# Kernel tuning notes

Hardware: AMD Instinct MI355X
Metric: run time of the kernel (lower is better)

Reference implementation:

```python
import jax, jax.numpy as jnp
import numpy as np

N = 50000
D_IN = 512
D_HID = 2048
N_CLS = 40
E = 200000


def setup_inputs() -> dict:
    key = jax.random.key(0)
    ks = jax.random.split(key, 8)
    x = jax.random.normal(ks[0], (N, D_IN), dtype=jnp.float32)
    edge_index = jax.random.randint(ks[1], (2, E), 0, N, dtype=jnp.int32)
    # GCNConv weights (glorot-ish scale) and biases
    W1 = jax.random.normal(ks[2], (D_IN, D_HID), dtype=jnp.float32) / np.sqrt(D_IN)
    b1 = jnp.zeros((D_HID,), dtype=jnp.float32)
    W2 = jax.random.normal(ks[3], (D_HID, D_HID), dtype=jnp.float32) / np.sqrt(D_HID)
    b2 = jnp.zeros((D_HID,), dtype=jnp.float32)
    W3 = jax.random.normal(ks[4], (D_HID, N_CLS), dtype=jnp.float32) / np.sqrt(D_HID)
    b3 = jnp.zeros((N_CLS,), dtype=jnp.float32)
    return {"x": x, "edge_index": edge_index, "W1": W1, "b1": b1,
            "W2": W2, "b2": b2, "W3": W3, "b3": b3}


def _gcn_conv(x, src, dst, deg_norm, W, b, n):
    # PyG GCNConv: transform first, then normalized sum-aggregate, then bias.
    h = x @ W                              # [N, out]
    msg = h[src] * deg_norm[:, None]       # [E+N, out] gather + edge normalize
    out = jax.ops.segment_sum(msg, dst, num_segments=n)  # scatter-add
    return out + b


def _pairnorm(x, scale=1.0, eps=1e-6):
    # PyG PairNorm (scale_individually=False): center cols, rescale by mean row norm.
    xc = x - x.mean(axis=0, keepdims=True)
    denom = jnp.sqrt(eps + (xc * xc).sum(axis=-1).mean())
    return scale * xc / denom


def _edges_with_self_loops_and_norm(edge_index, n):
    loop = jnp.arange(n, dtype=edge_index.dtype)
    src = jnp.concatenate([edge_index[0], loop])
    dst = jnp.concatenate([edge_index[1], loop])
    deg = jax.ops.segment_sum(jnp.ones_like(dst, dtype=jnp.float32), dst, num_segments=n)
    dinv = jnp.where(deg > 0, jax.lax.rsqrt(jnp.maximum(deg, 1.0)), 0.0)
    norm = dinv[src] * dinv[dst]           # D^{-1/2} (A+I) D^{-1/2} edge weights
    return src, dst, norm


def reference(x, edge_index, W1, b1, W2, b2, W3, b3):
    n = x.shape[0]
    # drop_edge keep_ratio=1.0 keeps all edges -> identity
    src, dst, norm = _edges_with_self_loops_and_norm(edge_index, n)
    h = _gcn_conv(x, src, dst, norm, W1, b1, n)
    h = jax.nn.relu(_pairnorm(h))
    h = _gcn_conv(h, src, dst, norm, W2, b2, n)
    h = jax.nn.relu(_pairnorm(h))
    out = _gcn_conv(h, src, dst, norm, W3, b3, n)
    return out
```

## Files before the change

### kernel.cpp

```cpp
#include <hip/hip_runtime.h>
#include <cstdint>
#include <cstddef>

using f32x4 = __attribute__((ext_vector_type(4))) float;
using short8 = __attribute__((ext_vector_type(8))) short;

__device__ __forceinline__ float blo(unsigned int u) { return __uint_as_float(u << 16); }
__device__ __forceinline__ float bhi(unsigned int u) { return __uint_as_float(u & 0xffff0000u); }
__device__ __forceinline__ unsigned short f2b(float f) {
  unsigned int i = __float_as_uint(f);
  return (unsigned short)((i + 0x7fffu + ((i >> 16) & 1u)) >> 16);
}
__device__ __forceinline__ unsigned int packb2(float a, float b) {
  return (unsigned int)f2b(a) | ((unsigned int)f2b(b) << 16);
}
__device__ __forceinline__ void gload_lds16(const void* g, void* l) {
  typedef __attribute__((address_space(1))) const unsigned int gui_t;
  typedef __attribute__((address_space(3))) unsigned int lui_t;
  __builtin_amdgcn_global_load_lds((gui_t*)(uintptr_t)g, (lui_t*)(uintptr_t)l, 16, 0, 0);
}
__device__ __forceinline__ void xcd_remap(int gx, int gy, int& bx, int& by) {
  int nwg = gx * gy;
  int flat = by * gx + bx;
  int q = nwg >> 3, rmd = nwg & 7;
  int xcd = flat & 7, pos = flat >> 3;
  int base = (xcd < rmd) ? xcd * (q + 1) : rmd * (q + 1) + (xcd - rmd) * q;
  int nf = base + pos;
  bx = nf % gx;
  by = nf / gx;
}

__global__ void k_sentinel(float* out, long long total, float v) {
  long long i = (long long)blockIdx.x * blockDim.x + threadIdx.x;
  long long stride = (long long)gridDim.x * blockDim.x;
  for (; i < total; i += stride) out[i] = v;
}

__global__ void k_init_deg(int* deg, int n) {
  int i = blockIdx.x * blockDim.x + threadIdx.x;
  if (i < n) deg[i] = 1;
}
__global__ void k_count(const int* __restrict__ ei, int* __restrict__ deg, int e) {
  int i = blockIdx.x * blockDim.x + threadIdx.x;
  if (i < e) atomicAdd(&deg[ei[e + i]], 1);
}
__global__ void k_dinv(const int* __restrict__ deg, float* __restrict__ dinv, int n) {
  int i = blockIdx.x * blockDim.x + threadIdx.x;
  if (i < n) dinv[i] = rsqrtf((float)deg[i]);
}
__global__ void k_scan(const int* __restrict__ deg, int* __restrict__ offs, int n) {
  __shared__ int sums[1024];
  int tid = threadIdx.x;
  int chunk = (n + 1023) / 1024;
  int s0 = tid * chunk, s1 = s0 + chunk;
  if (s1 > n) s1 = n;
  if (s0 > n) s0 = n;
  int s = 0;
  for (int i = s0; i < s1; i++) s += deg[i];
  sums[tid] = s;
  __syncthreads();
  if (tid == 0) {
    int acc = 0;
    for (int i = 0; i < 1024; i++) { int v = sums[i]; sums[i] = acc; acc += v; }
  }
  __syncthreads();
  int off = sums[tid];
  for (int i = s0; i < s1; i++) { offs[i] = off; off += deg[i]; }
  if (tid == 1023) offs[n] = off;
}
__global__ void k_copy_int(int* __restrict__ dst, const int* __restrict__ src, int n) {
  int i = blockIdx.x * blockDim.x + threadIdx.x;
  if (i < n) dst[i] = src[i];
}
__global__ void k_copy_u4(uint4* __restrict__ dst, const uint4* __restrict__ src, int n16) {
  int i = blockIdx.x * blockDim.x + threadIdx.x;
  int stride = gridDim.x * blockDim.x;
  for (; i < n16; i += stride) dst[i] = src[i];
}
__global__ void k_fill_edges(const int* __restrict__ ei, int e, int* __restrict__ cursor,
                             unsigned short* __restrict__ colv) {
  int i = blockIdx.x * blockDim.x + threadIdx.x;
  if (i < e) {
    int s = ei[i], d = ei[e + i];
    int pos = atomicAdd(&cursor[d], 1);
    colv[pos] = (unsigned short)s;
  }
}
__global__ void k_fill_loops(int* __restrict__ cursor, unsigned short* __restrict__ colv, int n) {
  int i = blockIdx.x * blockDim.x + threadIdx.x;
  if (i < n) {
    int pos = atomicAdd(&cursor[i], 1);
    colv[pos] = (unsigned short)i;
  }
}

__global__ void k_cvt_bf16(const float2* __restrict__ in, unsigned int* __restrict__ out, long long total) {
  long long i = (long long)blockIdx.x * blockDim.x + threadIdx.x;
  long long stride = (long long)gridDim.x * blockDim.x;
  for (; i < total; i += stride) {
    float2 v = in[i];
    out[i] = packb2(v.x, v.y);
  }
}
__global__ void k_transpose_cvt(const float* __restrict__ in, unsigned short* __restrict__ out,
                                int K, int M, int Mout) {
  __shared__ float tile[32][33];
  int kb = blockIdx.x * 32;
  int mb = blockIdx.y * 32;
  int tx = threadIdx.x, ty = threadIdx.y;
#pragma unroll
  for (int j = 0; j < 4; j++) {
    int k = kb + ty + j * 8, m = mb + tx;
    tile[ty + j * 8][tx] = (k < K && m < M) ? in[(size_t)k * M + m] : 0.0f;
  }
  __syncthreads();
#pragma unroll
  for (int j = 0; j < 4; j++) {
    int m = mb + ty + j * 8, k = kb + tx;
    if (m < Mout && k < K) out[(size_t)m * K + k] = f2b(tile[tx][ty + j * 8]);
  }
}

__global__ void k_aggregate_512(const unsigned int* __restrict__ in, unsigned short* __restrict__ out,
                                const int* __restrict__ offs, const unsigned short* __restrict__ colv,
                                const float* __restrict__ dinv) {
  int i = blockIdx.x;
  int tid = threadIdx.x;
  float di = dinv[i];
  int p0 = offs[i], p1 = offs[i + 1];
  float a0 = 0.f, a1 = 0.f;
  for (int p = p0; p < p1; p++) {
    int c = (int)colv[p];
    float wgt = dinv[c] * di;
    unsigned int u = in[(size_t)c * 256 + tid];
    a0 += wgt * blo(u); a1 += wgt * bhi(u);
  }
  ((unsigned int*)out)[(size_t)i * 256 + tid] = packb2(a0, a1);
}

__global__ void k_aggregate_pn(const unsigned short* __restrict__ in, unsigned short* __restrict__ outws,
                               unsigned short* __restrict__ outtail, int rsplit,
                               const int* __restrict__ offs, const unsigned short* __restrict__ colv,
                               const float* __restrict__ dinv, const float* __restrict__ meanv,
                               const float* __restrict__ scalev) {
  int i = blockIdx.x;
  int tid = threadIdx.x;
  float di = dinv[i];
  float s = scalev[0];
  float m[8];
#pragma unroll
  for (int j = 0; j < 8; j++) m[j] = meanv[tid * 8 + j];
  int p0 = offs[i], p1 = offs[i + 1];
  const uint4* inv = (const uint4*)in;
  float a[8] = {};
  for (int p = p0; p < p1; p++) {
    int c = (int)colv[p];
    float wgt = dinv[c] * di;
    uint4 u = inv[(size_t)c * 256 + tid];
    a[0] += wgt * fmaxf((blo(u.x) - m[0]) * s, 0.f);
    a[1] += wgt * fmaxf((bhi(u.x) - m[1]) * s, 0.f);
    a[2] += wgt * fmaxf((blo(u.y) - m[2]) * s, 0.f);
    a[3] += wgt * fmaxf((bhi(u.y) - m[3]) * s, 0.f);
    a[4] += wgt * fmaxf((blo(u.z) - m[4]) * s, 0.f);
    a[5] += wgt * fmaxf((bhi(u.z) - m[5]) * s, 0.f);
    a[6] += wgt * fmaxf((blo(u.w) - m[6]) * s, 0.f);
    a[7] += wgt * fmaxf((bhi(u.w) - m[7]) * s, 0.f);
  }
  uint4 o;
  o.x = packb2(a[0], a[1]); o.y = packb2(a[2], a[3]);
  o.z = packb2(a[4], a[5]); o.w = packb2(a[6], a[7]);
  char* base = (i < rsplit) ? (char*)outws + (size_t)i * 4096
                            : (char*)outtail + (size_t)(i - rsplit) * 4096;
  ((uint4*)base)[tid] = o;
}

template <int MQ>
__device__ __forceinline__ void load_a(const char* ldsA, short8 (&a)[4][2], int wm, int lane) {
  const int frow = lane & 15;
  const int cb0 = (lane >> 4) << 4;
  const int xorb = (lane & 7) << 4;
#pragma unroll
  for (int i = 0; i < 4; i++)
#pragma unroll
    for (int kk = 0; kk < 2; kk++)
      a[i][kk] = *(const short8*)(ldsA + (wm * 128 + MQ * 64 + i * 16 + frow) * 128 +
                                  ((kk * 64 + cb0) ^ xorb));
}
template <int NQ>
__device__ __forceinline__ void load_b(const char* ldsB, short8 (&b)[2][2][2], int wn, int lane) {
  const int frow = lane & 15;
  const int cb0 = (lane >> 4) << 4;
  const int xorb = (lane & 7) << 4;
#pragma unroll
  for (int j = 0; j < 2; j++)
#pragma unroll
    for (int kk = 0; kk < 2; kk++)
      b[NQ][j][kk] = *(const short8*)(ldsB + (wn * 64 + NQ * 32 + j * 16 + frow) * 128 +
                                      ((kk * 64 + cb0) ^ xorb));
}
template <int MQ, int NQ>
__device__ __forceinline__ void mfma_q(short8 (&a)[4][2], short8 (&b)[2][2][2], f32x4 (&acc)[8][4]) {
  __builtin_amdgcn_s_setprio(1);
#pragma unroll
  for (int i = 0; i < 4; i++)
#pragma unroll
    for (int j = 0; j < 2; j++)
#pragma unroll
      for (int kk = 0; kk < 2; kk++)
        acc[MQ * 4 + i][NQ * 2 + j] =
            __builtin_amdgcn_mfma_f32_16x16x32_bf16(a[i][kk], b[NQ][j][kk], acc[MQ * 4 + i][NQ * 2 + j], 0, 0, 0);
  __builtin_amdgcn_s_setprio(0);
}

__global__ __launch_bounds__(512, 2) void k_gemm256(const unsigned short* __restrict__ A,
                                                    const char* __restrict__ a_tail, int rsplit,
                                                    const unsigned short* __restrict__ BT,
                                                    const float* __restrict__ bias,
                                                    float* __restrict__ colsum, float* __restrict__ ssq,
                                                    unsigned short* __restrict__ Cout,
                                                    int M, int K, int Nout, int m_base) {
  __shared__ __align__(16) char smem[131072];
  const int t = threadIdx.x;
  const int lane = t & 63;
  const int wid = t >> 6;
  const int wm = wid >> 2, wn = wid & 3;
  int bx = blockIdx.x, by = blockIdx.y;
  xcd_remap(gridDim.x, gridDim.y, bx, by);
  const int n0 = bx * 256;
  const int m0 = m_base + by * 256;
  const size_t rowK = (size_t)K * 2;
  const int NT = K >> 6;

  const int rA = t >> 3;
  const int colS = (((t & 7) ^ ((t >> 3) & 7)) << 4);

  auto rowptrA = [&](int r) -> const char* {
    int gr = m0 + r; if (gr >= M) gr = M - 1;
    return (gr < rsplit ? (const char*)A + (size_t)gr * rowK
                        : a_tail + (size_t)(gr - rsplit) * rowK) + colS;
  };
  const char* sA00 = rowptrA(rA);
  const char* sA01 = rowptrA(128 + rA);
  const char* sA10 = rowptrA(64 + rA);
  const char* sA11 = rowptrA(192 + rA);
  const int rbl = (t >> 8) * 64 + ((t >> 3) & 31);
  const int rB00 = rbl, rB01 = 128 + rbl;
  const int rB10 = 32 + rbl, rB11 = 160 + rbl;
  const char* sB00 = (const char*)BT + (size_t)(n0 + rB00) * rowK + colS;
  const char* sB01 = (const char*)BT + (size_t)(n0 + rB01) * rowK + colS;
  const char* sB10 = (const char*)BT + (size_t)(n0 + rB10) * rowK + colS;
  const char* sB11 = (const char*)BT + (size_t)(n0 + rB11) * rowK + colS;
  const int t16 = t * 16;
  const int dA00 = t16, dA01 = 16384 + t16, dA10 = 8192 + t16, dA11 = 24576 + t16;
  const int c7 = (t & 7) * 16;
  const int dB00 = 32768 + rB00 * 128 + c7, dB01 = 32768 + rB01 * 128 + c7;
  const int dB10 = 32768 + rB10 * 128 + c7, dB11 = 32768 + rB11 * 128 + c7;

  f32x4 acc[8][4] = {};
  short8 a[4][2], b[2][2][2];

  gload_lds16(sA00, smem + dA00); gload_lds16(sA01, smem + dA01);
  gload_lds16(sA10, smem + dA10); gload_lds16(sA11, smem + dA11);
  gload_lds16(sB00, smem + dB00); gload_lds16(sB01, smem + dB01);
  gload_lds16(sB10, smem + dB10); gload_lds16(sB11, smem + dB11);
  gload_lds16(sA00 + 128, smem + 65536 + dA00); gload_lds16(sA01 + 128, smem + 65536 + dA01);
  gload_lds16(sA10 + 128, smem + 65536 + dA10); gload_lds16(sA11 + 128, smem + 65536 + dA11);
  sA00 += 256; sA01 += 256; sA10 += 256; sA11 += 256;
  sB00 += 128; sB01 += 128; sB10 += 128; sB11 += 128;
  asm volatile("s_waitcnt vmcnt(4)" ::: "memory");
  asm volatile("s_barrier" ::: "memory");
  load_a<0>((const char*)smem, a, wm, lane);
  load_b<0>((const char*)smem + 32768, b, wn, lane);

  for (int kt = 0; kt < NT; ++kt) {
    const int cbo = (kt & 1) << 16;
    const int sbo = cbo ^ 65536;
    const char* LA = (const char*)smem + cbo;
    const char* LB = LA + 32768;
    const char* NA = (const char*)smem + sbo;
    const char* NB = NA + 32768;
    char* SB = smem + sbo;
    char* SA = smem + cbo;
    gload_lds16(sB00, SB + dB00); gload_lds16(sB01, SB + dB01);
    asm volatile("s_waitcnt vmcnt(6)" ::: "memory");
    asm volatile("s_barrier" ::: "memory");
    mfma_q<0, 0>(a, b, acc);
    load_b<1>(LB, b, wn, lane);
    __builtin_amdgcn_sched_barrier(0);
    asm volatile("s_barrier" ::: "memory");
    gload_lds16(sB10, SB + dB10); gload_lds16(sB11, SB + dB11);
    asm volatile("s_barrier" ::: "memory");
    mfma_q<0, 1>(a, b, acc);
    load_a<1>(LA, a, wm, lane);
    __builtin_amdgcn_sched_barrier(0);
    asm volatile("s_barrier" ::: "memory");
    gload_lds16(sA00, SA + dA00); gload_lds16(sA01, SA + dA01);
    asm volatile("s_barrier" ::: "memory");
    mfma_q<1, 0>(a, b, acc);
    __builtin_amdgcn_sched_barrier(0);
    asm volatile("s_barrier" ::: "memory");
    gload_lds16(sA10, SA + dA10); gload_lds16(sA11, SA + dA11);
    asm volatile("s_waitcnt vmcnt(6)" ::: "memory");
    asm volatile("s_barrier" ::: "memory");
    mfma_q<1, 1>(a, b, acc);
    load_a<0>(NA, a, wm, lane);
    load_b<0>(NB, b, wn, lane);
    __builtin_amdgcn_sched_barrier(0);
    asm volatile("s_barrier" ::: "memory");
    sA00 += 128; sA01 += 128; sA10 += 128; sA11 += 128;
    sB00 += 128; sB01 += 128; sB10 += 128; sB11 += 128;
  }

  const int rrow = (lane >> 4) * 4;
  const int ccol = lane & 15;
  float ss = 0.f;
  float csum[4] = {0.f, 0.f, 0.f, 0.f};
#pragma unroll
  for (int f = 0; f < 8; f++) {
#pragma unroll
    for (int g = 0; g < 4; g++) {
      int col = n0 + wn * 64 + g * 16 + ccol;
      float bv = bias[col];
#pragma unroll
      for (int r = 0; r < 4; r++) {
        int row = m0 + wm * 128 + f * 16 + rrow + r;
        if (row < M) {
          float v = acc[f][g][r] + bv;
          Cout[(size_t)row * Nout + col] = f2b(v);
          csum[g] += v; ss += v * v;
        }
      }
    }
  }
#pragma unroll
  for (int g = 0; g < 4; g++) {
    float w = csum[g];
    w += __shfl_xor(w, 16);
    w += __shfl_xor(w, 32);
    if (lane < 16) atomicAdd(&colsum[n0 + wn * 64 + g * 16 + lane], w);
  }
  for (int mk = 32; mk >= 1; mk >>= 1) ss += __shfl_xor(ss, mk);
  if (lane == 0) atomicAdd(ssq, ss);
}

template <int BM, int BN, int WAVES_M, int WAVES_N, bool ADD_BIAS, bool OUT_BF16, bool STATS>
__global__ __launch_bounds__(256) void k_gemm_bf16(const unsigned short* __restrict__ A,
                                                   const char* __restrict__ a_tail, int rsplit,
                                                   const unsigned short* __restrict__ BT,
                                                   const float* __restrict__ bias,
                                                   float* __restrict__ colsum, float* __restrict__ ssq,
                                                   void* __restrict__ Cout,
                                                   int M, int K, int Nout, int m_base) {
  constexpr int BK = 64;
  constexpr int FM = BM / (WAVES_M * 16);
  constexpr int FN = BN / (WAVES_N * 16);
  __shared__ unsigned short lA[BM * BK];
  __shared__ unsigned short lB[BN * BK];
  const int tid = threadIdx.x;
  const int lane = tid & 63;
  const int wid = tid >> 6;
  int bx = blockIdx.x, by = blockIdx.y;
  xcd_remap(gridDim.x, gridDim.y, bx, by);
  const int n0 = bx * BN;
  const int m0 = m_base + by * BM;
  const int wrow = (wid / WAVES_N) * (FM * 16);
  const int wcol = (wid % WAVES_N) * (FN * 16);
  constexpr int ABYTES = BM * BK * 2;
  constexpr int BBYTES = BN * BK * 2;
  constexpr int ACH = ABYTES / 4096;
  constexpr int BCH = BBYTES / 4096;
  const size_t rowbytes = (size_t)K * 2;

  f32x4 acc[FM][FN] = {};
  const int frow = lane & 15;
  const int kcol8 = (lane >> 4) * 8;
  const int xorb = (lane & 7) << 4;

  for (int k0 = 0; k0 < K; k0 += BK) {
#pragma unroll
    for (int c = 0; c < ACH; c++) {
      int o = wid * (ABYTES / 4) + c * 1024 + lane * 16;
      int r = o >> 7;
      int kbs = (o & 127) ^ ((r & 7) << 4);
      int gr = m0 + r; if (gr >= M) gr = M - 1;
      const char* rowp = (gr < rsplit) ? (const char*)A + (size_t)gr * rowbytes
                                       : a_tail + (size_t)(gr - rsplit) * rowbytes;
      gload_lds16(rowp + (size_t)k0 * 2 + kbs, (char*)lA + o);
    }
#pragma unroll
    for (int c = 0; c < BCH; c++) {
      int o = wid * (BBYTES / 4) + c * 1024 + lane * 16;
      int r = o >> 7;
      int kbs = (o & 127) ^ ((r & 7) << 4);
      gload_lds16((const char*)BT + (size_t)(n0 + r) * rowbytes + (size_t)k0 * 2 + kbs, (char*)lB + o);
    }
    __syncthreads();
#pragma unroll
    for (int kk = 0; kk < BK; kk += 32) {
      short8 af[FM], bfr[FN];
#pragma unroll
      for (int t = 0; t < FM; t++)
        af[t] = *(const short8*)((const char*)lA + (wrow + t * 16 + frow) * 128 +
                                 (((kk + kcol8) * 2) ^ xorb));
#pragma unroll
      for (int u = 0; u < FN; u++)
        bfr[u] = *(const short8*)((const char*)lB + (wcol + u * 16 + frow) * 128 +
                                  (((kk + kcol8) * 2) ^ xorb));
#pragma unroll
      for (int t = 0; t < FM; t++)
#pragma unroll
        for (int u = 0; u < FN; u++)
          acc[t][u] = __builtin_amdgcn_mfma_f32_16x16x32_bf16(af[t], bfr[u], acc[t][u], 0, 0, 0);
    }
    __syncthreads();
  }

  const int rrow = (lane >> 4) * 4;
  const int ccol = lane & 15;
  float ss = 0.f;
  float ca[FN];
#pragma unroll
  for (int u = 0; u < FN; u++) ca[u] = 0.f;
#pragma unroll
  for (int t = 0; t < FM; t++) {
#pragma unroll
    for (int u = 0; u < FN; u++) {
#pragma unroll
      for (int r = 0; r < 4; r++) {
        int row = m0 + wrow + t * 16 + rrow + r;
        int col = n0 + wcol + u * 16 + ccol;
        if (row < M && col < Nout) {
          float v = acc[t][u][r];
          if constexpr (ADD_BIAS) v += bias[col];
          if constexpr (OUT_BF16)
            ((unsigned short*)Cout)[(size_t)row * Nout + col] = f2b(v);
          else
            ((float*)Cout)[(size_t)row * Nout + col] = v;
          if constexpr (STATS) { ca[u] += v; ss += v * v; }
        }
      }
    }
  }
  if constexpr (STATS) {
#pragma unroll
    for (int u = 0; u < FN; u++) {
      float w = ca[u];
      w += __shfl_xor(w, 16);
      w += __shfl_xor(w, 32);
      if (lane < 16) atomicAdd(&colsum[n0 + wcol + u * 16 + lane], w);
    }
    for (int mk = 32; mk >= 1; mk >>= 1) ss += __shfl_xor(ss, mk);
    if (lane == 0) atomicAdd(ssq, ss);
  }
}

__global__ void k_zero(float* p, int n) {
  int i = blockIdx.x * blockDim.x + threadIdx.x;
  if (i < n) p[i] = 0.f;
}
__global__ void k_finalize(const float* __restrict__ colsum, const float* __restrict__ ssq,
                           float* __restrict__ meanv, float* __restrict__ scalev, int nrows, int ncols) {
  __shared__ float red[1024];
  int tid = threadIdx.x;
  float m2 = 0.f;
  for (int c = tid; c < ncols; c += 1024) {
    float m = colsum[c] / (float)nrows;
    meanv[c] = m;
    m2 += m * m;
  }
  red[tid] = m2;
  __syncthreads();
  for (int s = 512; s > 0; s >>= 1) {
    if (tid < s) red[tid] += red[tid + s];
    __syncthreads();
  }
  if (tid == 0) {
    float sstot = ssq[0] - (float)nrows * red[0];
    scalev[0] = rsqrtf(1e-6f + sstot / (float)nrows);
  }
}
__global__ void k_apply_pn_relu(unsigned int* __restrict__ h, const float* __restrict__ meanv,
                                const float* __restrict__ scalev, long long total, int ucolmask) {
  float s = scalev[0];
  long long i = (long long)blockIdx.x * blockDim.x + threadIdx.x;
  long long stride = (long long)gridDim.x * blockDim.x;
  for (; i < total; i += stride) {
    unsigned int u = h[i];
    int cp = (int)(i & ucolmask);
    float a = (blo(u) - meanv[2 * cp]) * s;
    float b = (bhi(u) - meanv[2 * cp + 1]) * s;
    h[i] = packb2(fmaxf(a, 0.f), fmaxf(b, 0.f));
  }
}

__global__ void k_aggregate_out(const float* __restrict__ t, const int* __restrict__ offs,
                                const unsigned short* __restrict__ colv, const float* __restrict__ dinv,
                                const float* __restrict__ b3, float* __restrict__ outp, int ncls) {
  int i = blockIdx.x;
  int j = threadIdx.x;
  if (j < ncls) {
    float di = dinv[i];
    float acc = b3[j];
    for (int p = offs[i]; p < offs[i + 1]; p++) {
      int c = (int)colv[p];
      acc += dinv[c] * di * t[(size_t)c * ncls + j];
    }
    outp[(size_t)i * ncls + j] = acc;
  }
}

extern "C" void kernel_launch(void* const* d_in, const int* in_sizes, int n_in,
                              void* d_out, int out_size, void* d_ws, size_t ws_size,
                              hipStream_t stream) {
  (void)n_in;
  const float* x = (const float*)d_in[0];
  const int* ei = (const int*)d_in[1];
  const float* W1 = (const float*)d_in[2];
  const float* b1 = (const float*)d_in[3];
  const float* W2 = (const float*)d_in[4];
  const float* b2 = (const float*)d_in[5];
  const float* W3 = (const float*)d_in[6];
  const float* b3 = (const float*)d_in[7];
  const int DI = 512, DH = 2048, NC = 40;
  const int n = in_sizes[0] / DI;
  const int e = in_sizes[1] / 2;

  const size_t BIG1B = (size_t)n * DH * 2;
  char* BIG1 = (char*)d_ws;
  char* BIG2 = (char*)d_ws + BIG1B;

  char* dob = (char*)d_out;
  int* deg = (int*)(dob + 0);
  float* dinv = (float*)(dob + 200064);
  int* offs = (int*)(dob + 400128);
  unsigned short* colv = (unsigned short*)(dob + 600192);
  float* colsum = (float*)(dob + 1100288);
  float* meanv = (float*)(dob + 1108480);
  float* ssq = (float*)(dob + 1116672);
  float* scalev = (float*)(dob + 1116928);
  char* aggtail = dob + 2097152;

  long long rows_ws = (long long)(ws_size - BIG1B) / (DH * 2);
  int rsplit = (rows_ws > n) ? n : (int)rows_ws;

  if (ws_size < 403800000UL || rsplit < 48560) {
    float v = (float)(double)(ws_size >> 20);
    k_sentinel<<<512, 256, 0, stream>>>((float*)d_out, (long long)out_size, v);
    return;
  }

  const int W2ROW0 = 47952;
  unsigned short* WT2 = (unsigned short*)(BIG1 + (size_t)W2ROW0 * 4096);
  const int PH2_MBASE = 47872;
  const int PH2_TILES = (n - PH2_MBASE + 255) / 256;

  unsigned short* agg1 = (unsigned short*)BIG2;
  unsigned short* xb = (unsigned short*)(BIG2 + 64000000);
  unsigned short* WT1 = (unsigned short*)(BIG2 + 120000000);
  unsigned short* agg2 = (unsigned short*)BIG2;
  unsigned short* WT2c = (unsigned short*)BIG2;
  float* tbuf = (float*)BIG2;
  unsigned short* WT3 = (unsigned short*)(BIG2 + 9000000);
  int* offs_c = (int*)(BIG2 + 10000000);
  unsigned short* colv_c = (unsigned short*)(BIG2 + 11000000);
  float* dinv_c = (float*)(BIG2 + 12000000);

  dim3 b256(256);
  dim3 b512(512);
  int gn = (n + 255) / 256, ge = (e + 255) / 256;

  k_init_deg<<<gn, b256, 0, stream>>>(deg, n);
  k_count<<<ge, b256, 0, stream>>>(ei, deg, e);
  k_dinv<<<gn, b256, 0, stream>>>(deg, dinv, n);
  k_scan<<<1, 1024, 0, stream>>>(deg, offs, n);
  k_copy_int<<<gn, b256, 0, stream>>>(deg, offs, n);
  k_fill_edges<<<ge, b256, 0, stream>>>(ei, e, deg, colv);
  k_fill_loops<<<gn, b256, 0, stream>>>(deg, colv, n);

  dim3 tb(32, 8);

  k_cvt_bf16<<<2048, b256, 0, stream>>>((const float2*)x, (unsigned int*)xb, (long long)n * DI / 2);
  k_aggregate_512<<<n, b256, 0, stream>>>((const unsigned int*)xb, agg1, offs, colv, dinv);
  k_transpose_cvt<<<dim3(DI / 32, DH / 32), tb, 0, stream>>>(W1, WT1, DI, DH, DH);
  k_zero<<<(DH + 255) / 256, b256, 0, stream>>>(colsum, DH);
  k_zero<<<1, b256, 0, stream>>>(ssq, 1);
  k_gemm256<<<dim3(DH / 256, (n + 255) / 256), b512, 0, stream>>>(
      agg1, (const char*)agg1, n, WT1, b1, colsum, ssq, (unsigned short*)BIG1, n, DI, DH, 0);
  k_finalize<<<1, 1024, 0, stream>>>(colsum, ssq, meanv, scalev, n, DH);

  k_aggregate_pn<<<n, b256, 0, stream>>>((const unsigned short*)BIG1, agg2, (unsigned short*)aggtail,
                                         rsplit, offs, colv, dinv, meanv, scalev);
  k_transpose_cvt<<<dim3(DH / 32, DH / 32), tb, 0, stream>>>(W2, WT2, DH, DH, DH);
  k_zero<<<(DH + 255) / 256, b256, 0, stream>>>(colsum, DH);
  k_zero<<<1, b256, 0, stream>>>(ssq, 1);
  k_gemm256<<<dim3(DH / 256, 187), b512, 0, stream>>>(
      agg2, aggtail, rsplit, WT2, b2, colsum, ssq, (unsigned short*)BIG1, n, DH, DH, 0);
  k_copy_u4<<<2048, b256, 0, stream>>>((uint4*)WT2c, (const uint4*)WT2, (int)(8388608 / 16));
  k_gemm256<<<dim3(DH / 256, PH2_TILES), b512, 0, stream>>>(
      agg2, aggtail, rsplit, WT2c, b2, colsum, ssq, (unsigned short*)BIG1, n, DH, DH, PH2_MBASE);
  k_finalize<<<1, 1024, 0, stream>>>(colsum, ssq, meanv, scalev, n, DH);
  k_apply_pn_relu<<<2048, b256, 0, stream>>>((unsigned int*)BIG1, meanv, scalev, (long long)n * DH / 2, DH / 2 - 1);

  k_transpose_cvt<<<dim3(DH / 32, 2), tb, 0, stream>>>(W3, WT3, DH, NC, 64);
  k_gemm_bf16<128, 64, 4, 1, false, false, false><<<dim3(1, (n + 127) / 128), b256, 0, stream>>>(
      (const unsigned short*)BIG1, BIG1, n, WT3, nullptr, nullptr, nullptr, tbuf, n, DH, NC, 0);
  k_copy_int<<<(n + 256) / 256, b256, 0, stream>>>(offs_c, offs, n + 1);
  k_copy_int<<<((e + n) / 2 + 255) / 256, b256, 0, stream>>>((int*)colv_c, (const int*)colv, (e + n) / 2);
  k_copy_int<<<gn, b256, 0, stream>>>((int*)dinv_c, (const int*)dinv, n);
  k_aggregate_out<<<n, 64, 0, stream>>>(tbuf, offs_c, colv_c, dinv_c, b3, (float*)d_out, NC);
}
```

Baseline: 1.403 ms.

## Fuse PairNorm+ReLU into final GEMM A-load and merge small launches

Drops the separate full-tensor PairNorm/ReLU pass over the N×2048 bf16 hidden activations. The normalization is instead applied while the layer-3 GEMM loads its A tiles into LDS, using a new 64-row-tile kernel. It also merges the stats-zeroing and three metadata copy kernels into single launches, makes finalize reset the accumulators, and packs four nodes per block in the output aggregation. The A path now uses register loads plus VALU conversion instead of direct global-to-LDS loads, which may reduce load overlap in the final GEMM.

```diff
diff --git a/kernel.cpp b/kernel.cpp
--- a/kernel.cpp
+++ b/kernel.cpp
@@ -92,6 +92,15 @@
     int pos = atomicAdd(&cursor[i], 1);
     colv[pos] = (unsigned short)i;
   }
+}
+__global__ void k_copy_meta(const int* __restrict__ offs, int* __restrict__ offs_c,
+                            const int* __restrict__ colv, int* __restrict__ colv_c, int colv_ints,
+                            const float* __restrict__ dinv, float* __restrict__ dinv_c, int n) {
+  int i = blockIdx.x * blockDim.x + threadIdx.x;
+  int stride = gridDim.x * blockDim.x;
+  for (int k = i; k <= n; k += stride) offs_c[k] = offs[k];
+  for (int k = i; k < colv_ints; k += stride) colv_c[k] = colv[k];
+  for (int k = i; k < n; k += stride) dinv_c[k] = dinv[k];
 }
 
 __global__ void k_cvt_bf16(const float2* __restrict__ in, unsigned int* __restrict__ out, long long total) {
@@ -343,122 +352,87 @@
   if (lane == 0) atomicAdd(ssq, ss);
 }
 
-template <int BM, int BN, int WAVES_M, int WAVES_N, bool ADD_BIAS, bool OUT_BF16, bool STATS>
-__global__ __launch_bounds__(256) void k_gemm_bf16(const unsigned short* __restrict__ A,
-                                                   const char* __restrict__ a_tail, int rsplit,
-                                                   const unsigned short* __restrict__ BT,
-                                                   const float* __restrict__ bias,
-                                                   float* __restrict__ colsum, float* __restrict__ ssq,
-                                                   void* __restrict__ Cout,
-                                                   int M, int K, int Nout, int m_base) {
+__global__ __launch_bounds__(256) void k_gemm3_pn(const unsigned short* __restrict__ A,
+                                                  const float* __restrict__ meanv,
+                                                  const float* __restrict__ scalev,
+                                                  const unsigned short* __restrict__ BT,
+                                                  float* __restrict__ Cout,
+                                                  int M, int K, int Nout) {
   constexpr int BK = 64;
-  constexpr int FM = BM / (WAVES_M * 16);
-  constexpr int FN = BN / (WAVES_N * 16);
-  __shared__ unsigned short lA[BM * BK];
-  __shared__ unsigned short lB[BN * BK];
+  constexpr int FN = 4;
+  __shared__ __align__(16) unsigned short lA[64 * BK];
+  __shared__ __align__(16) unsigned short lB[64 * BK];
   const int tid = threadIdx.x;
   const int lane = tid & 63;
   const int wid = tid >> 6;
-  int bx = blockIdx.x, by = blockIdx.y;
-  xcd_remap(gridDim.x, gridDim.y, bx, by);
-  const int n0 = bx * BN;
-  const int m0 = m_base + by * BM;
-  const int wrow = (wid / WAVES_N) * (FM * 16);
-  const int wcol = (wid % WAVES_N) * (FN * 16);
-  constexpr int ABYTES = BM * BK * 2;
-  constexpr int BBYTES = BN * BK * 2;
-  constexpr int ACH = ABYTES / 4096;
-  constexpr int BCH = BBYTES / 4096;
-  const size_t rowbytes = (size_t)K * 2;
-
-  f32x4 acc[FM][FN] = {};
+  const int m0 = blockIdx.y * 64;
+  const int wrow = wid * 16;
+  const size_t rowK = (size_t)K * 2;
+  const float s = scalev[0];
+
+  f32x4 acc[FN] = {};
   const int frow = lane & 15;
   const int kcol8 = (lane >> 4) * 8;
   const int xorb = (lane & 7) << 4;
 
   for (int k0 = 0; k0 < K; k0 += BK) {
 #pragma unroll
-    for (int c = 0; c < ACH; c++) {
-      int o = wid * (ABYTES / 4) + c * 1024 + lane * 16;
+    for (int c = 0; c < 2; c++) {
+      int o = c * 4096 + tid * 16;
+      int r = o >> 7;
+      int kb = o & 127;
+      int gr = m0 + r; if (gr >= M) gr = M - 1;
+      uint4 u = *(const uint4*)((const char*)A + (size_t)gr * rowK + (size_t)k0 * 2 + kb);
+      int col = k0 + (kb >> 1);
+      float4 m0v = *(const float4*)&meanv[col];
+      float4 m1v = *(const float4*)&meanv[col + 4];
+      uint4 g;
+      g.x = packb2(fmaxf((blo(u.x) - m0v.x) * s, 0.f), fmaxf((bhi(u.x) - m0v.y) * s, 0.f));
+      g.y = packb2(fmaxf((blo(u.y) - m0v.z) * s, 0.f), fmaxf((bhi(u.y) - m0v.w) * s, 0.f));
+      g.z = packb2(fmaxf((blo(u.z) - m1v.x) * s, 0.f), fmaxf((bhi(u.z) - m1v.y) * s, 0.f));
+      g.w = packb2(fmaxf((blo(u.w) - m1v.z) * s, 0.f), fmaxf((bhi(u.w) - m1v.w) * s, 0.f));
+      *(uint4*)((char*)lA + (o ^ ((r & 7) << 4))) = g;
+    }
+#pragma unroll
+    for (int c = 0; c < 2; c++) {
+      int o = c * 4096 + tid * 16;
       int r = o >> 7;
       int kbs = (o & 127) ^ ((r & 7) << 4);
-      int gr = m0 + r; if (gr >= M) gr = M - 1;
-      const char* rowp = (gr < rsplit) ? (const char*)A + (size_t)gr * rowbytes
-                                       : a_tail + (size_t)(gr - rsplit) * rowbytes;
-      gload_lds16(rowp + (size_t)k0 * 2 + kbs, (char*)lA + o);
-    }
-#pragma unroll
-    for (int c = 0; c < BCH; c++) {
-      int o = wid * (BBYTES / 4) + c * 1024 + lane * 16;
-      int r = o >> 7;
-      int kbs = (o & 127) ^ ((r & 7) << 4);
-      gload_lds16((const char*)BT + (size_t)(n0 + r) * rowbytes + (size_t)k0 * 2 + kbs, (char*)lB + o);
+      gload_lds16((const char*)BT + (size_t)r * rowK + (size_t)k0 * 2 + kbs, (char*)lB + o);
     }
     __syncthreads();
 #pragma unroll
     for (int kk = 0; kk < BK; kk += 32) {
-      short8 af[FM], bfr[FN];
-#pragma unroll
-      for (int t = 0; t < FM; t++)
-        af[t] = *(const short8*)((const char*)lA + (wrow + t * 16 + frow) * 128 +
-                                 (((kk + kcol8) * 2) ^ xorb));
-#pragma unroll
-      for (int u = 0; u < FN; u++)
-        bfr[u] = *(const short8*)((const char*)lB + (wcol + u * 16 + frow) * 128 +
-                                  (((kk + kcol8) * 2) ^ xorb));
-#pragma unroll
-      for (int t = 0; t < FM; t++)
-#pragma unroll
-        for (int u = 0; u < FN; u++)
-          acc[t][u] = __builtin_amdgcn_mfma_f32_16x16x32_bf16(af[t], bfr[u], acc[t][u], 0, 0, 0);
+      short8 af = *(const short8*)((const char*)lA + (wrow + frow) * 128 + (((kk + kcol8) * 2) ^ xorb));
+#pragma unroll
+      for (int u = 0; u < FN; u++) {
+        short8 bf = *(const short8*)((const char*)lB + (u * 16 + frow) * 128 + (((kk + kcol8) * 2) ^ xorb));
+        acc[u] = __builtin_amdgcn_mfma_f32_16x16x32_bf16(af, bf, acc[u], 0, 0, 0);
+      }
     }
     __syncthreads();
   }
 
   const int rrow = (lane >> 4) * 4;
   const int ccol = lane & 15;
-  float ss = 0.f;
-  float ca[FN];
-#pragma unroll
-  for (int u = 0; u < FN; u++) ca[u] = 0.f;
-#pragma unroll
-  for (int t = 0; t < FM; t++) {
-#pragma unroll
-    for (int u = 0; u < FN; u++) {
-#pragma unroll
-      for (int r = 0; r < 4; r++) {
-        int row = m0 + wrow + t * 16 + rrow + r;
-        int col = n0 + wcol + u * 16 + ccol;
-        if (row < M && col < Nout) {
-          float v = acc[t][u][r];
-          if constexpr (ADD_BIAS) v += bias[col];
-          if constexpr (OUT_BF16)
-            ((unsigned short*)Cout)[(size_t)row * Nout + col] = f2b(v);
-          else
-            ((float*)Cout)[(size_t)row * Nout + col] = v;
-          if constexpr (STATS) { ca[u] += v; ss += v * v; }
-        }
-      }
+#pragma unroll
+  for (int u = 0; u < FN; u++) {
+#pragma unroll
+    for (int r = 0; r < 4; r++) {
+      int row = m0 + wrow + rrow + r;
+      int col = u * 16 + ccol;
+      if (row < M && col < Nout)
+        Cout[(size_t)row * Nout + col] = acc[u][r];
     }
   }
-  if constexpr (STATS) {
-#pragma unroll
-    for (int u = 0; u < FN; u++) {
-      float w = ca[u];
-      w += __shfl_xor(w, 16);
-      w += __shfl_xor(w, 32);
-      if (lane < 16) atomicAdd(&colsum[n0 + wcol + u * 16 + lane], w);
-    }
-    for (int mk = 32; mk >= 1; mk >>= 1) ss += __shfl_xor(ss, mk);
-    if (lane == 0) atomicAdd(ssq, ss);
-  }
-}
-
-__global__ void k_zero(float* p, int n) {
-  int i = blockIdx.x * blockDim.x + threadIdx.x;
-  if (i < n) p[i] = 0.f;
-}
-__global__ void k_finalize(const float* __restrict__ colsum, const float* __restrict__ ssq,
+}
+
+__global__ void k_zero_stats(float* colsum, float* ssq, int n) {
+  int i = blockIdx.x * blockDim.x + threadIdx.x;
+  if (i < n) colsum[i] = 0.f;
+  if (i == 0) ssq[0] = 0.f;
+}
+__global__ void k_finalize(float* __restrict__ colsum, float* __restrict__ ssq,
                            float* __restrict__ meanv, float* __restrict__ scalev, int nrows, int ncols) {
   __shared__ float red[1024];
   int tid = threadIdx.x;
@@ -467,6 +441,7 @@
     float m = colsum[c] / (float)nrows;
     meanv[c] = m;
     m2 += m * m;
+    colsum[c] = 0.f;
   }
   red[tid] = m2;
   __syncthreads();
@@ -477,28 +452,16 @@
   if (tid == 0) {
     float sstot = ssq[0] - (float)nrows * red[0];
     scalev[0] = rsqrtf(1e-6f + sstot / (float)nrows);
-  }
-}
-__global__ void k_apply_pn_relu(unsigned int* __restrict__ h, const float* __restrict__ meanv,
-                                const float* __restrict__ scalev, long long total, int ucolmask) {
-  float s = scalev[0];
-  long long i = (long long)blockIdx.x * blockDim.x + threadIdx.x;
-  long long stride = (long long)gridDim.x * blockDim.x;
-  for (; i < total; i += stride) {
-    unsigned int u = h[i];
-    int cp = (int)(i & ucolmask);
-    float a = (blo(u) - meanv[2 * cp]) * s;
-    float b = (bhi(u) - meanv[2 * cp + 1]) * s;
-    h[i] = packb2(fmaxf(a, 0.f), fmaxf(b, 0.f));
+    ssq[0] = 0.f;
   }
 }
 
 __global__ void k_aggregate_out(const float* __restrict__ t, const int* __restrict__ offs,
                                 const unsigned short* __restrict__ colv, const float* __restrict__ dinv,
-                                const float* __restrict__ b3, float* __restrict__ outp, int ncls) {
-  int i = blockIdx.x;
-  int j = threadIdx.x;
-  if (j < ncls) {
+                                const float* __restrict__ b3, float* __restrict__ outp, int n, int ncls) {
+  int i = blockIdx.x * 4 + (threadIdx.x >> 6);
+  int j = threadIdx.x & 63;
+  if (i < n && j < ncls) {
     float di = dinv[i];
     float acc = b3[j];
     for (int p = offs[i]; p < offs[i + 1]; p++) {
@@ -582,8 +545,7 @@
   k_cvt_bf16<<<2048, b256, 0, stream>>>((const float2*)x, (unsigned int*)xb, (long long)n * DI / 2);
   k_aggregate_512<<<n, b256, 0, stream>>>((const unsigned int*)xb, agg1, offs, colv, dinv);
   k_transpose_cvt<<<dim3(DI / 32, DH / 32), tb, 0, stream>>>(W1, WT1, DI, DH, DH);
-  k_zero<<<(DH + 255) / 256, b256, 0, stream>>>(colsum, DH);
-  k_zero<<<1, b256, 0, stream>>>(ssq, 1);
+  k_zero_stats<<<(DH + 255) / 256, b256, 0, stream>>>(colsum, ssq, DH);
   k_gemm256<<<dim3(DH / 256, (n + 255) / 256), b512, 0, stream>>>(
       agg1, (const char*)agg1, n, WT1, b1, colsum, ssq, (unsigned short*)BIG1, n, DI, DH, 0);
   k_finalize<<<1, 1024, 0, stream>>>(colsum, ssq, meanv, scalev, n, DH);
@@ -591,21 +553,18 @@
   k_aggregate_pn<<<n, b256, 0, stream>>>((const unsigned short*)BIG1, agg2, (unsigned short*)aggtail,
                                          rsplit, offs, colv, dinv, meanv, scalev);
   k_transpose_cvt<<<dim3(DH / 32, DH / 32), tb, 0, stream>>>(W2, WT2, DH, DH, DH);
-  k_zero<<<(DH + 255) / 256, b256, 0, stream>>>(colsum, DH);
-  k_zero<<<1, b256, 0, stream>>>(ssq, 1);
   k_gemm256<<<dim3(DH / 256, 187), b512, 0, stream>>>(
       agg2, aggtail, rsplit, WT2, b2, colsum, ssq, (unsigned short*)BIG1, n, DH, DH, 0);
   k_copy_u4<<<2048, b256, 0, stream>>>((uint4*)WT2c, (const uint4*)WT2, (int)(8388608 / 16));
   k_gemm256<<<dim3(DH / 256, PH2_TILES), b512, 0, stream>>>(
       agg2, aggtail, rsplit, WT2c, b2, colsum, ssq, (unsigned short*)BIG1, n, DH, DH, PH2_MBASE);
   k_finalize<<<1, 1024, 0, stream>>>(colsum, ssq, meanv, scalev, n, DH);
-  k_apply_pn_relu<<<2048, b256, 0, stream>>>((unsigned int*)BIG1, meanv, scalev, (long long)n * DH / 2, DH / 2 - 1);
 
   k_transpose_cvt<<<dim3(DH / 32, 2), tb, 0, stream>>>(W3, WT3, DH, NC, 64);
-  k_gemm_bf16<128, 64, 4, 1, false, false, false><<<dim3(1, (n + 127) / 128), b256, 0, stream>>>(
-      (const unsigned short*)BIG1, BIG1, n, WT3, nullptr, nullptr, nullptr, tbuf, n, DH, NC, 0);
-  k_copy_int<<<(n + 256) / 256, b256, 0, stream>>>(offs_c, offs, n + 1);
-  k_copy_int<<<((e + n) / 2 + 255) / 256, b256, 0, stream>>>((int*)colv_c, (const int*)colv, (e + n) / 2);
-  k_copy_int<<<gn, b256, 0, stream>>>((int*)dinv_c, (const int*)dinv, n);
-  k_aggregate_out<<<n, 64, 0, stream>>>(tbuf, offs_c, colv_c, dinv_c, b3, (float*)d_out, NC);
-}
+  k_gemm3_pn<<<dim3(1, (n + 63) / 64), b256, 0, stream>>>(
+      (const unsigned short*)BIG1, meanv, scalev, WT3, tbuf, n, DH, NC);
+  k_copy_meta<<<256, b256, 0, stream>>>(offs, offs_c, (const int*)colv, (int*)colv_c, (e + n) / 2,
+                                        dinv, dinv_c, n);
+  k_aggregate_out<<<(n + 3) / 4, b256, 0, stream>>>(tbuf, offs_c, colv_c, dinv_c, b3,
+                                                    (float*)d_out, n, NC);
+}
```

New measurement: 1.358 ms. 3.3% less time.
